# Kernel optimization log

Measured on AMD Instinct MI355X. Metric: run time of the kernel, lower is better.

## Reference

```python
import jax, jax.numpy as jnp
import numpy as np

HIDDEN = 256
GROUPS = 4
GDIM = HIDDEN // GROUPS  # 64


def setup_inputs() -> dict:
    key = jax.random.key(0)
    k1, k2, k3, k4 = jax.random.split(key, 4)
    B, N, P = 8, 300, 32
    x = jax.random.normal(k1, (B, N, P, HIDDEN), dtype=jnp.float32)
    query_content = jax.random.normal(k2, (B, N, HIDDEN), dtype=jnp.float32)
    out_dim = GDIM * GDIM * GROUPS
    # nn.Linear default init: U(-1/sqrt(fan_in), 1/sqrt(fan_in))
    bound = 1.0 / np.sqrt(HIDDEN)
    W_gen = jax.random.uniform(k3, (HIDDEN, out_dim), dtype=jnp.float32, minval=-bound, maxval=bound)
    b_gen = jax.random.uniform(k4, (out_dim,), dtype=jnp.float32, minval=-bound, maxval=bound)
    gamma = jnp.ones((HIDDEN,), dtype=jnp.float32)
    beta = jnp.zeros((HIDDEN,), dtype=jnp.float32)
    return {"x": x, "query_content": query_content, "W_gen": W_gen, "b_gen": b_gen, "gamma": gamma, "beta": beta}


def _layer_norm(h, gamma, beta, eps=1e-5):
    mu = jnp.mean(h, axis=-1, keepdims=True)
    var = jnp.var(h, axis=-1, keepdims=True)
    return (h - mu) * jax.lax.rsqrt(var + eps) * gamma + beta


def reference(x, query_content, W_gen, b_gen, gamma, beta):
    B, N, P, C = x.shape
    # dynamic per-query weights: [B,N,G,gd,gd]
    w = (query_content @ W_gen + b_gen).reshape(B, N, GROUPS, GDIM, GDIM)
    xg = x.reshape(B, N, P, GROUPS, GDIM)
    # mixed[...,p,g,e] = sum_d xg[...,p,g,d] * w[...,g,e,d]  (matmul with W^T)
    mixed = jnp.einsum('bnpgd,bnged->bnpge', xg, w).reshape(B, N, P, C)
    return jax.nn.relu(_layer_norm(mixed, gamma, beta))
```

## Files before the change

### kernel.cpp

```cpp
#include <hip/hip_runtime.h>
#include <hip/hip_bf16.h>

typedef __attribute__((ext_vector_type(4))) float floatx4;
typedef __attribute__((ext_vector_type(8))) short short8;

#define HIDDEN 256
#define NOUT 16384

__device__ __forceinline__ short bf16bits(float x) {
    __hip_bfloat16 h = __float2bfloat16(x);
    return __builtin_bit_cast(short, h);
}

#define GLDS16(gsrc, ldst) \
    __builtin_amdgcn_global_load_lds((const __attribute__((address_space(1))) void*)(gsrc), \
                                     (__attribute__((address_space(3))) void*)(ldst), 16, 0, 0)

__global__ __launch_bounds__(256) void kC(const float* __restrict__ src, short* __restrict__ dst, int n4)
{
    int i = blockIdx.x * 256 + threadIdx.x;
    if (i >= n4) return;
    float4 f = reinterpret_cast<const float4*>(src)[i];
    short4 v;
    v.x = bf16bits(f.x); v.y = bf16bits(f.y); v.z = bf16bits(f.z); v.w = bf16bits(f.w);
    reinterpret_cast<short4*>(dst)[i] = v;
}

__global__ __launch_bounds__(256) void kT(const float* __restrict__ Wg, short* __restrict__ WgT)
{
    __shared__ short t[64 * 68];
    const int tid = threadIdx.x;
    const int n0 = blockIdx.x * 64, k0 = blockIdx.y * 64;

    const int r  = tid >> 4;
    const int c4 = tid & 15;
    #pragma unroll
    for (int i = 0; i < 4; ++i) {
        const int kl = r + i * 16;
        float4 f = *reinterpret_cast<const float4*>(Wg + (size_t)(k0 + kl) * NOUT + n0 + c4 * 4);
        short4 v;
        v.x = bf16bits(f.x); v.y = bf16bits(f.y); v.z = bf16bits(f.z); v.w = bf16bits(f.w);
        *reinterpret_cast<short4*>(&t[kl * 68 + c4 * 4]) = v;
    }
    __syncthreads();

    #pragma unroll
    for (int h = 0; h < 2; ++h) {
        const int id = tid + h * 256;
        const int nl = id >> 3, kc = id & 7;
        short8 v;
        #pragma unroll
        for (int j = 0; j < 8; ++j) v[j] = t[(kc * 8 + j) * 68 + nl];
        *reinterpret_cast<short8*>(WgT + (size_t)(n0 + nl) * HIDDEN + k0 + kc * 8) = v;
    }
}

__global__ __launch_bounds__(256) void kA2(
    const short* __restrict__ qcb, const short* __restrict__ WgT,
    const float* __restrict__ bg, short* __restrict__ wdyn, int M)
{
    __shared__ short As[128 * 32];
    __shared__ short Bs[128 * 32];

    const int tid  = threadIdx.x;
    const int wave = tid >> 6, lane = tid & 63;
    const int lq   = lane & 15, quad = lane >> 4;
    const int wm   = wave >> 1, wn = wave & 1;
    const int m0   = blockIdx.y * 128;
    const int n0   = blockIdx.x * 128;

    const int ml = lane >> 2;
    const int kq = (lane & 3) ^ ((lane >> 3) & 3);

    int rowA0 = m0 + wave * 32 + ml;       if (rowA0 >= M) rowA0 = M - 1;
    int rowA1 = m0 + wave * 32 + 16 + ml;  if (rowA1 >= M) rowA1 = M - 1;
    const int rowB0 = n0 + wave * 32 + ml;
    const int rowB1 = rowB0 + 16;
    const short* aSrc0 = qcb + (size_t)rowA0 * HIDDEN + kq * 8;
    const short* aSrc1 = qcb + (size_t)rowA1 * HIDDEN + kq * 8;
    const short* bSrc0 = WgT + (size_t)rowB0 * HIDDEN + kq * 8;
    const short* bSrc1 = WgT + (size_t)rowB1 * HIDDEN + kq * 8;
    short* aDst0 = &As[(wave * 32) * 32];
    short* aDst1 = &As[(wave * 32 + 16) * 32];
    short* bDst0 = &Bs[(wave * 32) * 32];
    short* bDst1 = &Bs[(wave * 32 + 16) * 32];

    const int kswz = quad ^ ((lq >> 1) & 3);
    const short* aFrag[4];
    const short* bFrag[4];
    #pragma unroll
    for (int i = 0; i < 4; ++i) {
        aFrag[i] = &As[(wm * 64 + i * 16 + lq) * 32 + kswz * 8];
        bFrag[i] = &Bs[(wn * 64 + i * 16 + lq) * 32 + kswz * 8];
    }

    floatx4 acc[4][4];
    #pragma unroll
    for (int i = 0; i < 4; ++i)
        #pragma unroll
        for (int j = 0; j < 4; ++j) acc[i][j] = (floatx4){0.f, 0.f, 0.f, 0.f};

    for (int k0 = 0; k0 < HIDDEN; k0 += 32) {
        GLDS16(aSrc0, aDst0);
        GLDS16(aSrc1, aDst1);
        GLDS16(bSrc0, bDst0);
        GLDS16(bSrc1, bDst1);
        aSrc0 += 32; aSrc1 += 32; bSrc0 += 32; bSrc1 += 32;
        __syncthreads();

        short8 a[4], b[4];
        #pragma unroll
        for (int i = 0; i < 4; ++i) a[i] = *reinterpret_cast<const short8*>(aFrag[i]);
        #pragma unroll
        for (int j = 0; j < 4; ++j) b[j] = *reinterpret_cast<const short8*>(bFrag[j]);
        #pragma unroll
        for (int i = 0; i < 4; ++i)
            #pragma unroll
            for (int j = 0; j < 4; ++j)
                acc[i][j] = __builtin_amdgcn_mfma_f32_16x16x32_bf16(a[i], b[j], acc[i][j], 0, 0, 0);
        __syncthreads();
    }

    #pragma unroll
    for (int j = 0; j < 4; ++j) {
        const int col = n0 + wn * 64 + j * 16 + lq;
        const float bv = bg[col];
        #pragma unroll
        for (int i = 0; i < 4; ++i) {
            const int rbase = m0 + wm * 64 + i * 16 + quad * 4;
            #pragma unroll
            for (int r = 0; r < 4; ++r) {
                const int row = rbase + r;
                if (row < M) wdyn[(size_t)row * NOUT + col] = bf16bits(acc[i][j][r] + bv);
            }
        }
    }
}

__global__ __launch_bounds__(256) void kB2(
    const float* __restrict__ x, const short* __restrict__ wdyn,
    const float* __restrict__ gamma, const float* __restrict__ beta,
    float* __restrict__ out)
{
    __shared__ float red[2][4][4][2][2];

    const int tid  = threadIdx.x;
    const int bnq  = blockIdx.x;
    const int wave = tid >> 6, lane = tid & 63;
    const int lq   = lane & 15, quad = lane >> 4;
    const int mtile = wave & 1, gp = wave >> 1;

    const float* xr = x + (size_t)bnq * (32 * HIDDEN) + (mtile * 16 + lq) * HIDDEN;
    const short* wr = wdyn + (size_t)bnq * NOUT;

    short8 afr[2][2];
    #pragma unroll
    for (int gi = 0; gi < 2; ++gi) {
        const int g = gp * 2 + gi;
        #pragma unroll
        for (int ks = 0; ks < 2; ++ks) {
            const float4* s = reinterpret_cast<const float4*>(xr + g * 64 + ks * 32 + quad * 8);
            const float4 f0 = s[0], f1 = s[1];
            short8 v;
            v[0]=bf16bits(f0.x); v[1]=bf16bits(f0.y); v[2]=bf16bits(f0.z); v[3]=bf16bits(f0.w);
            v[4]=bf16bits(f1.x); v[5]=bf16bits(f1.y); v[6]=bf16bits(f1.z); v[7]=bf16bits(f1.w);
            afr[gi][ks] = v;
        }
    }

    floatx4 acc[2][4];
    #pragma unroll
    for (int gi = 0; gi < 2; ++gi)
        #pragma unroll
        for (int nt = 0; nt < 4; ++nt) acc[gi][nt] = (floatx4){0.f, 0.f, 0.f, 0.f};

    #pragma unroll
    for (int gi = 0; gi < 2; ++gi) {
        const int g = gp * 2 + gi;
        #pragma unroll
        for (int ks = 0; ks < 2; ++ks) {
            #pragma unroll
            for (int nt = 0; nt < 4; ++nt) {
                const short8 b = *reinterpret_cast<const short8*>(
                    wr + (g * 64 + nt * 16 + lq) * 64 + ks * 32 + quad * 8);
                acc[gi][nt] = __builtin_amdgcn_mfma_f32_16x16x32_bf16(afr[gi][ks], b, acc[gi][nt], 0, 0, 0);
            }
        }
    }

    float s[4], ss[4];
    #pragma unroll
    for (int r = 0; r < 4; ++r) { s[r] = 0.f; ss[r] = 0.f; }
    #pragma unroll
    for (int gi = 0; gi < 2; ++gi)
        #pragma unroll
        for (int nt = 0; nt < 4; ++nt)
            #pragma unroll
            for (int r = 0; r < 4; ++r) {
                const float v = acc[gi][nt][r];
                s[r] += v; ss[r] += v * v;
            }
    #pragma unroll
    for (int off = 1; off < 16; off <<= 1) {
        #pragma unroll
        for (int r = 0; r < 4; ++r) {
            s[r]  += __shfl_xor(s[r],  off);
            ss[r] += __shfl_xor(ss[r], off);
        }
    }
    if (lq == 0) {
        #pragma unroll
        for (int r = 0; r < 4; ++r) {
            red[mtile][quad][r][gp][0] = s[r];
            red[mtile][quad][r][gp][1] = ss[r];
        }
    }
    __syncthreads();

    float mu[4], rs[4];
    #pragma unroll
    for (int r = 0; r < 4; ++r) {
        const float S  = s[r]  + red[mtile][quad][r][gp ^ 1][0];
        const float SS = ss[r] + red[mtile][quad][r][gp ^ 1][1];
        mu[r] = S * (1.f / 256.f);
        float var = SS * (1.f / 256.f) - mu[r] * mu[r];
        var = fmaxf(var, 0.f);
        rs[r] = rsqrtf(var + 1e-5f);
    }

    float* orow = out + (size_t)bnq * (32 * HIDDEN);
    #pragma unroll
    for (int gi = 0; gi < 2; ++gi) {
        const int g = gp * 2 + gi;
        #pragma unroll
        for (int nt = 0; nt < 4; ++nt) {
            const int c = g * 64 + nt * 16 + lq;
            const float gm = gamma[c], bt = beta[c];
            #pragma unroll
            for (int r = 0; r < 4; ++r) {
                const int p = mtile * 16 + quad * 4 + r;
                const float v = fmaxf((acc[gi][nt][r] - mu[r]) * rs[r] * gm + bt, 0.f);
                orow[p * HIDDEN + c] = v;
            }
        }
    }
}

extern "C" void kernel_launch(void* const* d_in, const int* in_sizes, int n_in,
                              void* d_out, int out_size, void* d_ws, size_t ws_size,
                              hipStream_t stream)
{
    const float* x     = (const float*)d_in[0];
    const float* qc    = (const float*)d_in[1];
    const float* Wg    = (const float*)d_in[2];
    const float* bg    = (const float*)d_in[3];
    const float* gamma = (const float*)d_in[4];
    const float* beta  = (const float*)d_in[5];
    float* out = (float*)d_out;

    const int M = in_sizes[1] / HIDDEN;

    char* ws = (char*)d_ws;
    short* wdyn = (short*)ws;
    short* WgT  = (short*)(ws + (size_t)M * NOUT * 2);
    short* qcb  = (short*)(ws + (size_t)M * NOUT * 2 + (size_t)NOUT * HIDDEN * 2);

    {
        const int n4 = (M * HIDDEN) / 4;
        kC<<<(n4 + 255) / 256, 256, 0, stream>>>(qc, qcb, n4);
    }
    kT<<<dim3(NOUT / 64, HIDDEN / 64), 256, 0, stream>>>(Wg, WgT);
    kA2<<<dim3(NOUT / 128, (M + 127) / 128), 256, 0, stream>>>(qcb, WgT, bg, wdyn, M);
    kB2<<<M, 256, 0, stream>>>(x, wdyn, gamma, beta, out);
}
```

Before: 252.3 us.

## Merge prep kernels, deepen GEMM K-tile, stage output via LDS, use nontemporal I/O

Combines the qc bf16 conversion and the W_gen transpose into a single prep launch. The weight-generation GEMM now loads 64-wide K tiles with an XOR swizzle and swaps grid axes so M varies fastest for better reuse of W tiles. Its epilogue is staged through LDS so the bf16 dynamic weights are written as coalesced 16-byte stores. The mixing kernel uses nontemporal loads for x and wdyn and nontemporal stores for the output, to avoid polluting the cache with streaming data. Costs are more LDS per block and extra barriers in the epilogue.

Result: faster. 237.6 us (-5.8%).

```diff
diff --git a/kernel.cpp b/kernel.cpp
--- a/kernel.cpp
+++ b/kernel.cpp
@@ -7,7 +7,7 @@
 #define HIDDEN 256
 #define NOUT 16384
 
-__device__ __forceinline__ short bf16bits(float x) {
+static __device__ __forceinline__ short bf16bits(float x) {
     __hip_bfloat16 h = __float2bfloat16(x);
     return __builtin_bit_cast(short, h);
 }
@@ -16,83 +16,84 @@
     __builtin_amdgcn_global_load_lds((const __attribute__((address_space(1))) void*)(gsrc), \
                                      (__attribute__((address_space(3))) void*)(ldst), 16, 0, 0)
 
-__global__ __launch_bounds__(256) void kC(const float* __restrict__ src, short* __restrict__ dst, int n4)
-{
-    int i = blockIdx.x * 256 + threadIdx.x;
-    if (i >= n4) return;
-    float4 f = reinterpret_cast<const float4*>(src)[i];
-    short4 v;
-    v.x = bf16bits(f.x); v.y = bf16bits(f.y); v.z = bf16bits(f.z); v.w = bf16bits(f.w);
-    reinterpret_cast<short4*>(dst)[i] = v;
-}
-
-__global__ __launch_bounds__(256) void kT(const float* __restrict__ Wg, short* __restrict__ WgT)
+__global__ __launch_bounds__(256) void kPrep(
+    const float* __restrict__ Wg, short* __restrict__ WgT,
+    const float* __restrict__ qc, short* __restrict__ qcb, int n4)
 {
     __shared__ short t[64 * 68];
     const int tid = threadIdx.x;
-    const int n0 = blockIdx.x * 64, k0 = blockIdx.y * 64;
-
-    const int r  = tid >> 4;
-    const int c4 = tid & 15;
-    #pragma unroll
-    for (int i = 0; i < 4; ++i) {
-        const int kl = r + i * 16;
-        float4 f = *reinterpret_cast<const float4*>(Wg + (size_t)(k0 + kl) * NOUT + n0 + c4 * 4);
-        short4 v;
-        v.x = bf16bits(f.x); v.y = bf16bits(f.y); v.z = bf16bits(f.z); v.w = bf16bits(f.w);
-        *reinterpret_cast<short4*>(&t[kl * 68 + c4 * 4]) = v;
-    }
-    __syncthreads();
-
-    #pragma unroll
-    for (int h = 0; h < 2; ++h) {
-        const int id = tid + h * 256;
-        const int nl = id >> 3, kc = id & 7;
-        short8 v;
-        #pragma unroll
-        for (int j = 0; j < 8; ++j) v[j] = t[(kc * 8 + j) * 68 + nl];
-        *reinterpret_cast<short8*>(WgT + (size_t)(n0 + nl) * HIDDEN + k0 + kc * 8) = v;
-    }
-}
-
-__global__ __launch_bounds__(256) void kA2(
+
+    if (blockIdx.x < 1024) {
+        const int n0 = (blockIdx.x & 255) * 64, k0 = (blockIdx.x >> 8) * 64;
+        const int r  = tid >> 4;
+        const int c4 = tid & 15;
+        #pragma unroll
+        for (int i = 0; i < 4; ++i) {
+            const int kl = r + i * 16;
+            float4 f = *reinterpret_cast<const float4*>(Wg + (size_t)(k0 + kl) * NOUT + n0 + c4 * 4);
+            short4 v;
+            v.x = bf16bits(f.x); v.y = bf16bits(f.y); v.z = bf16bits(f.z); v.w = bf16bits(f.w);
+            *reinterpret_cast<short4*>(&t[kl * 68 + c4 * 4]) = v;
+        }
+        __syncthreads();
+        #pragma unroll
+        for (int h = 0; h < 2; ++h) {
+            const int id = tid + h * 256;
+            const int nl = id >> 3, kc = id & 7;
+            short8 v;
+            #pragma unroll
+            for (int j = 0; j < 8; ++j) v[j] = t[(kc * 8 + j) * 68 + nl];
+            *reinterpret_cast<short8*>(WgT + (size_t)(n0 + nl) * HIDDEN + k0 + kc * 8) = v;
+        }
+    } else {
+        const int i = (blockIdx.x - 1024) * 256 + tid;
+        if (i < n4) {
+            float4 f = reinterpret_cast<const float4*>(qc)[i];
+            short4 v;
+            v.x = bf16bits(f.x); v.y = bf16bits(f.y); v.z = bf16bits(f.z); v.w = bf16bits(f.w);
+            reinterpret_cast<short4*>(qcb)[i] = v;
+        }
+    }
+}
+
+__global__ __launch_bounds__(256) void kA3(
     const short* __restrict__ qcb, const short* __restrict__ WgT,
     const float* __restrict__ bg, short* __restrict__ wdyn, int M)
 {
-    __shared__ short As[128 * 32];
-    __shared__ short Bs[128 * 32];
+    __shared__ short As[128 * 64];
+    __shared__ short Bs[128 * 64];
 
     const int tid  = threadIdx.x;
     const int wave = tid >> 6, lane = tid & 63;
     const int lq   = lane & 15, quad = lane >> 4;
     const int wm   = wave >> 1, wn = wave & 1;
-    const int m0   = blockIdx.y * 128;
-    const int n0   = blockIdx.x * 128;
-
-    const int ml = lane >> 2;
-    const int kq = (lane & 3) ^ ((lane >> 3) & 3);
-
-    int rowA0 = m0 + wave * 32 + ml;       if (rowA0 >= M) rowA0 = M - 1;
-    int rowA1 = m0 + wave * 32 + 16 + ml;  if (rowA1 >= M) rowA1 = M - 1;
-    const int rowB0 = n0 + wave * 32 + ml;
-    const int rowB1 = rowB0 + 16;
-    const short* aSrc0 = qcb + (size_t)rowA0 * HIDDEN + kq * 8;
-    const short* aSrc1 = qcb + (size_t)rowA1 * HIDDEN + kq * 8;
-    const short* bSrc0 = WgT + (size_t)rowB0 * HIDDEN + kq * 8;
-    const short* bSrc1 = WgT + (size_t)rowB1 * HIDDEN + kq * 8;
-    short* aDst0 = &As[(wave * 32) * 32];
-    short* aDst1 = &As[(wave * 32 + 16) * 32];
-    short* bDst0 = &Bs[(wave * 32) * 32];
-    short* bDst1 = &Bs[(wave * 32 + 16) * 32];
-
-    const int kswz = quad ^ ((lq >> 1) & 3);
-    const short* aFrag[4];
-    const short* bFrag[4];
-    #pragma unroll
-    for (int i = 0; i < 4; ++i) {
-        aFrag[i] = &As[(wm * 64 + i * 16 + lq) * 32 + kswz * 8];
-        bFrag[i] = &Bs[(wn * 64 + i * 16 + lq) * 32 + kswz * 8];
-    }
+    const int m0   = blockIdx.x * 128;
+    const int n0   = blockIdx.y * 128;
+
+    const short* aSrc[4]; const short* bSrc[4];
+    short* aDst[4]; short* bDst[4];
+    #pragma unroll
+    for (int t = 0; t < 4; ++t) {
+        const int chunk = t * 256 + wave * 64 + lane;
+        const int row = chunk >> 3, kc = chunk & 7;
+        const int kcs = kc ^ (row & 7);
+        int rA = m0 + row; if (rA >= M) rA = M - 1;
+        aSrc[t] = qcb + (size_t)rA * HIDDEN + kcs * 8;
+        bSrc[t] = WgT + (size_t)(n0 + row) * HIDDEN + kcs * 8;
+        aDst[t] = &As[(t * 256 + wave * 64) * 8];
+        bDst[t] = &Bs[(t * 256 + wave * 64) * 8];
+    }
+
+    int aOff[2][4], bOff[2][4];
+    #pragma unroll
+    for (int ks = 0; ks < 2; ++ks)
+        #pragma unroll
+        for (int i = 0; i < 4; ++i) {
+            const int ra = wm * 64 + i * 16 + lq;
+            aOff[ks][i] = ra * 64 + (((ks * 4 + quad) ^ (ra & 7)) * 8);
+            const int rb = wn * 64 + i * 16 + lq;
+            bOff[ks][i] = rb * 64 + (((ks * 4 + quad) ^ (rb & 7)) * 8);
+        }
 
     floatx4 acc[4][4];
     #pragma unroll
@@ -100,44 +101,63 @@
         #pragma unroll
         for (int j = 0; j < 4; ++j) acc[i][j] = (floatx4){0.f, 0.f, 0.f, 0.f};
 
-    for (int k0 = 0; k0 < HIDDEN; k0 += 32) {
-        GLDS16(aSrc0, aDst0);
-        GLDS16(aSrc1, aDst1);
-        GLDS16(bSrc0, bDst0);
-        GLDS16(bSrc1, bDst1);
-        aSrc0 += 32; aSrc1 += 32; bSrc0 += 32; bSrc1 += 32;
-        __syncthreads();
-
-        short8 a[4], b[4];
-        #pragma unroll
-        for (int i = 0; i < 4; ++i) a[i] = *reinterpret_cast<const short8*>(aFrag[i]);
-        #pragma unroll
-        for (int j = 0; j < 4; ++j) b[j] = *reinterpret_cast<const short8*>(bFrag[j]);
-        #pragma unroll
-        for (int i = 0; i < 4; ++i)
+    for (int it = 0; it < 4; ++it) {
+        #pragma unroll
+        for (int t = 0; t < 4; ++t) {
+            GLDS16(aSrc[t], aDst[t]);
+            GLDS16(bSrc[t], bDst[t]);
+            aSrc[t] += 64; bSrc[t] += 64;
+        }
+        __syncthreads();
+
+        #pragma unroll
+        for (int ks = 0; ks < 2; ++ks) {
+            short8 a[4], b[4];
+            #pragma unroll
+            for (int i = 0; i < 4; ++i) a[i] = *reinterpret_cast<const short8*>(&As[aOff[ks][i]]);
+            #pragma unroll
+            for (int j = 0; j < 4; ++j) b[j] = *reinterpret_cast<const short8*>(&Bs[bOff[ks][j]]);
+            #pragma unroll
+            for (int i = 0; i < 4; ++i)
+                #pragma unroll
+                for (int j = 0; j < 4; ++j)
+                    acc[i][j] = __builtin_amdgcn_mfma_f32_16x16x32_bf16(a[i], b[j], acc[i][j], 0, 0, 0);
+        }
+        __syncthreads();
+    }
+
+    float bv[4];
+    #pragma unroll
+    for (int j = 0; j < 4; ++j) bv[j] = bg[n0 + wn * 64 + j * 16 + lq];
+
+    short* Cs = As;
+    #pragma unroll
+    for (int half = 0; half < 2; ++half) {
+        if (half) __syncthreads();
+        if (wm == half) {
             #pragma unroll
             for (int j = 0; j < 4; ++j)
-                acc[i][j] = __builtin_amdgcn_mfma_f32_16x16x32_bf16(a[i], b[j], acc[i][j], 0, 0, 0);
-        __syncthreads();
-    }
-
-    #pragma unroll
-    for (int j = 0; j < 4; ++j) {
-        const int col = n0 + wn * 64 + j * 16 + lq;
-        const float bv = bg[col];
-        #pragma unroll
-        for (int i = 0; i < 4; ++i) {
-            const int rbase = m0 + wm * 64 + i * 16 + quad * 4;
-            #pragma unroll
-            for (int r = 0; r < 4; ++r) {
-                const int row = rbase + r;
-                if (row < M) wdyn[(size_t)row * NOUT + col] = bf16bits(acc[i][j][r] + bv);
-            }
-        }
-    }
-}
-
-__global__ __launch_bounds__(256) void kB2(
+                #pragma unroll
+                for (int i = 0; i < 4; ++i)
+                    #pragma unroll
+                    for (int r = 0; r < 4; ++r)
+                        Cs[(i * 16 + quad * 4 + r) * 128 + wn * 64 + j * 16 + lq] =
+                            bf16bits(acc[i][j][r] + bv[j]);
+        }
+        __syncthreads();
+        #pragma unroll
+        for (int t = 0; t < 4; ++t) {
+            const int id = t * 256 + tid;
+            const int mr = id >> 4, ch = id & 15;
+            const int grow = m0 + half * 64 + mr;
+            if (grow < M)
+                *reinterpret_cast<short8*>(&wdyn[(size_t)grow * NOUT + n0 + ch * 8]) =
+                    *reinterpret_cast<const short8*>(&Cs[mr * 128 + ch * 8]);
+        }
+    }
+}
+
+__global__ __launch_bounds__(256) void kB3(
     const float* __restrict__ x, const short* __restrict__ wdyn,
     const float* __restrict__ gamma, const float* __restrict__ beta,
     float* __restrict__ out)
@@ -159,11 +179,12 @@
         const int g = gp * 2 + gi;
         #pragma unroll
         for (int ks = 0; ks < 2; ++ks) {
-            const float4* s = reinterpret_cast<const float4*>(xr + g * 64 + ks * 32 + quad * 8);
-            const float4 f0 = s[0], f1 = s[1];
+            const floatx4* s = reinterpret_cast<const floatx4*>(xr + g * 64 + ks * 32 + quad * 8);
+            const floatx4 f0 = __builtin_nontemporal_load(s);
+            const floatx4 f1 = __builtin_nontemporal_load(s + 1);
             short8 v;
-            v[0]=bf16bits(f0.x); v[1]=bf16bits(f0.y); v[2]=bf16bits(f0.z); v[3]=bf16bits(f0.w);
-            v[4]=bf16bits(f1.x); v[5]=bf16bits(f1.y); v[6]=bf16bits(f1.z); v[7]=bf16bits(f1.w);
+            v[0]=bf16bits(f0[0]); v[1]=bf16bits(f0[1]); v[2]=bf16bits(f0[2]); v[3]=bf16bits(f0[3]);
+            v[4]=bf16bits(f1[0]); v[5]=bf16bits(f1[1]); v[6]=bf16bits(f1[2]); v[7]=bf16bits(f1[3]);
             afr[gi][ks] = v;
         }
     }
@@ -181,8 +202,8 @@
         for (int ks = 0; ks < 2; ++ks) {
             #pragma unroll
             for (int nt = 0; nt < 4; ++nt) {
-                const short8 b = *reinterpret_cast<const short8*>(
-                    wr + (g * 64 + nt * 16 + lq) * 64 + ks * 32 + quad * 8);
+                const short8 b = __builtin_nontemporal_load(reinterpret_cast<const short8*>(
+                    wr + (g * 64 + nt * 16 + lq) * 64 + ks * 32 + quad * 8));
                 acc[gi][nt] = __builtin_amdgcn_mfma_f32_16x16x32_bf16(afr[gi][ks], b, acc[gi][nt], 0, 0, 0);
             }
         }
@@ -240,7 +261,7 @@
             for (int r = 0; r < 4; ++r) {
                 const int p = mtile * 16 + quad * 4 + r;
                 const float v = fmaxf((acc[gi][nt][r] - mu[r]) * rs[r] * gm + bt, 0.f);
-                orow[p * HIDDEN + c] = v;
+                __builtin_nontemporal_store(v, &orow[p * HIDDEN + c]);
             }
         }
     }
@@ -265,11 +286,11 @@
     short* WgT  = (short*)(ws + (size_t)M * NOUT * 2);
     short* qcb  = (short*)(ws + (size_t)M * NOUT * 2 + (size_t)NOUT * HIDDEN * 2);
 
-    {
-        const int n4 = (M * HIDDEN) / 4;
-        kC<<<(n4 + 255) / 256, 256, 0, stream>>>(qc, qcb, n4);
-    }
-    kT<<<dim3(NOUT / 64, HIDDEN / 64), 256, 0, stream>>>(Wg, WgT);
-    kA2<<<dim3(NOUT / 128, (M + 127) / 128), 256, 0, stream>>>(qcb, WgT, bg, wdyn, M);
-    kB2<<<M, 256, 0, stream>>>(x, wdyn, gamma, beta, out);
-}
+    const int n4 = (M * HIDDEN) / 4;
+    const int prepBlocks = 1024 + (n4 + 255) / 256;
+    kPrep<<<prepBlocks, 256, 0, stream>>>(Wg, WgT, qc, qcb, n4);
+
+    kA3<<<dim3((M + 127) / 128, NOUT / 128), 256, 0, stream>>>(qcb, WgT, bg, wdyn, M);
+
+    kB3<<<M, 256, 0, stream>>>(x, wdyn, gamma, beta, out);
+}
```
